# Kernel optimization log

Hardware: AMD Instinct MI355X
Metric: run time of the kernel (lower is better)

Reference implementation:

```python
import jax, jax.numpy as jnp
import numpy as np

N_NODES = 100000
N_EDGES = 1600000
IN_C, HID_C, OUT_C = 128, 128, 64


def setup_inputs() -> dict:
    key = jax.random.key(0)
    k1, k2, k3, k4 = jax.random.split(key, 4)
    x = jax.random.normal(k1, (N_NODES, IN_C), dtype=jnp.float32)
    edge_index = jax.random.randint(k2, (2, N_EDGES), 0, N_NODES, dtype=jnp.int32)
    # Glorot-ish init for linear weights, zero bias (PyG GCNConv default bias=0)
    W1 = jax.random.normal(k3, (IN_C, HID_C), dtype=jnp.float32) / np.sqrt(IN_C)
    b1 = jnp.zeros((HID_C,), dtype=jnp.float32)
    W2 = jax.random.normal(k4, (HID_C, OUT_C), dtype=jnp.float32) / np.sqrt(HID_C)
    b2 = jnp.zeros((OUT_C,), dtype=jnp.float32)
    return {"x": x, "edge_index": edge_index, "W1": W1, "b1": b1, "W2": W2, "b2": b2}


def gcn_conv(x, edge_index, W, b, n_nodes):
    """PyG GCNConv: out = D^{-1/2} (A + I) D^{-1/2} (x W) + b."""
    h = x @ W  # [N, C_out]
    loop = jnp.arange(n_nodes, dtype=edge_index.dtype)
    src = jnp.concatenate([edge_index[0], loop])  # messages flow src -> dst
    dst = jnp.concatenate([edge_index[1], loop])
    # degree at destination nodes (includes self-loops)
    deg = jax.ops.segment_sum(jnp.ones_like(src, dtype=h.dtype), dst,
                              num_segments=n_nodes)
    dis = jnp.where(deg > 0, jax.lax.rsqrt(jnp.maximum(deg, 1e-12)), 0.0)
    norm = dis[src] * dis[dst]  # [E+N]
    msg = h[src] * norm[:, None]  # gather + scale
    out = jax.ops.segment_sum(msg, dst, num_segments=n_nodes)  # scatter-add
    return out + b


def reference(x, edge_index, W1, b1, W2, b2):
    h = jax.nn.relu(gcn_conv(x, edge_index, W1, b1, N_NODES))
    return gcn_conv(h, edge_index, W2, b2, N_NODES)
```

## Files before the change

### kernel.cpp

```cpp
#include <hip/hip_runtime.h>

#define N_NODES 100000
#define N_EDGES 1600000
#define IN_C 128
#define HID_C 128
#define OUT_C 64

#define SH 8
#define NBKT 391
#define CAP 4608
#define EPB 4096
#define EPT 16

typedef __attribute__((ext_vector_type(8))) short bf16x8;
typedef __attribute__((ext_vector_type(4))) float f32x4;

static __device__ __forceinline__ unsigned f2bf(float f) {
  union { float f; unsigned u; } v; v.f = f;
  unsigned r = v.u + 0x7fffu + ((v.u >> 16) & 1u);
  return r >> 16;
}
static __device__ __forceinline__ float bf2f(unsigned hu) {
  union { unsigned u; float f; } v; v.u = hu << 16; return v.f;
}
static __device__ __forceinline__ float bflo(unsigned u) {
  union { unsigned u; float f; } v; v.u = u << 16; return v.f;
}
static __device__ __forceinline__ float bfhi(unsigned u) {
  union { unsigned u; float f; } v; v.u = u & 0xffff0000u; return v.f;
}


__global__ __launch_bounds__(256) void k_partA(const int* __restrict__ src,
                                               const int* __restrict__ dst,
                                               int* __restrict__ bcnt,
                                               unsigned* __restrict__ tmp, int e) {
  __shared__ unsigned stage[EPB];
  __shared__ unsigned short bid[EPB];
  __shared__ int hist[NBKT];
  __shared__ int lstart[NBKT];
  __shared__ int base[NBKT];
  __shared__ int ps[256];
  const int t = threadIdx.x;
  const int e0 = blockIdx.x * EPB;
  const int m = (e0 + EPB < e ? EPB : e - e0);

  for (int i = t; i < NBKT; i += 256) hist[i] = 0;
  __syncthreads();

  int rsrc[EPT], rdst[EPT];
#pragma unroll
  for (int i = 0; i < EPT; ++i) {
    int idx = e0 + i * 256 + t;
    if (idx < e) {
      rsrc[i] = src[idx];
      rdst[i] = dst[idx];
      atomicAdd(&hist[rdst[i] >> SH], 1);
    }
  }
  __syncthreads();

  int a0 = (2 * t < NBKT) ? hist[2 * t] : 0;
  int a1 = (2 * t + 1 < NBKT) ? hist[2 * t + 1] : 0;
  ps[t] = a0 + a1;
  __syncthreads();
  for (int off = 1; off < 256; off <<= 1) {
    int add = (t >= off) ? ps[t - off] : 0;
    __syncthreads();
    ps[t] += add;
    __syncthreads();
  }
  int ex = ps[t] - (a0 + a1);
  if (2 * t < NBKT) lstart[2 * t] = ex;
  if (2 * t + 1 < NBKT) lstart[2 * t + 1] = ex + a0;

  for (int i = t; i < NBKT; i += 256) {
    int h = hist[i];
    base[i] = h ? atomicAdd(&bcnt[i], h) : 0;
    hist[i] = 0;
  }
  __syncthreads();

#pragma unroll
  for (int i = 0; i < EPT; ++i) {
    int idx = e0 + i * 256 + t;
    if (idx < e) {
      int d = rdst[i];
      int b = d >> SH;
      int pos = lstart[b] + atomicAdd(&hist[b], 1);
      stage[pos] = (unsigned)rsrc[i] | ((unsigned)(d & 255) << 17);
      bid[pos] = (unsigned short)b;
    }
  }
  __syncthreads();

  for (int pos = t; pos < m; pos += 256) {
    int b = bid[pos];
    int slot = base[b] + (pos - lstart[b]);
    if (slot < CAP)
      tmp[(size_t)b * CAP + slot] = stage[pos];
  }
}

__global__ __launch_bounds__(256) void k_cntb(const unsigned* __restrict__ tmp,
                                              const int* __restrict__ bcnt,
                                              int* __restrict__ cnt, int n) {
  __shared__ int h[256];
  const int b = blockIdx.x, t = threadIdx.x;
  h[t] = 0;
  __syncthreads();
  int m = bcnt[b];
  if (m > CAP) m = CAP;
  for (int j = t; j < m; j += 256)
    atomicAdd(&h[tmp[(size_t)b * CAP + j] >> 17], 1);
  __syncthreads();
  int node = (b << SH) + t;
  if (node < n) cnt[node] = h[t];
}

__global__ void k_scan_block(const int* __restrict__ cnt, int* __restrict__ rowptr,
                             int* __restrict__ bsums, float* __restrict__ dis, int n) {
  __shared__ int s[256];
  int t = threadIdx.x;
  int i = blockIdx.x * 256 + t;
  int v = (i < n) ? cnt[i] : 0;
  if (i < n) dis[i] = rsqrtf((float)(v + 1));
  s[t] = v;
  __syncthreads();
  for (int off = 1; off < 256; off <<= 1) {
    int add = (t >= off) ? s[t - off] : 0;
    __syncthreads();
    s[t] += add;
    __syncthreads();
  }
  if (i < n) rowptr[i] = s[t] - v;
  if (t == 255) bsums[blockIdx.x] = s[255];
}

__global__ void k_scan_sums(int* __restrict__ bsums, int nb) {
  __shared__ int s[512];
  int t = threadIdx.x;
  int v = (t < nb) ? bsums[t] : 0;
  s[t] = v;
  __syncthreads();
  for (int off = 1; off < 512; off <<= 1) {
    int add = (t >= off) ? s[t - off] : 0;
    __syncthreads();
    s[t] += add;
    __syncthreads();
  }
  if (t < nb) bsums[t] = s[t] - v;
}

__global__ void k_add_off(int* __restrict__ rowptr, const int* __restrict__ bsums,
                          int n, int e) {
  int i = blockIdx.x * blockDim.x + threadIdx.x;
  if (i < n) rowptr[i] += bsums[i >> 8];
  else if (i == n) rowptr[n] = e;
}

__global__ __launch_bounds__(256) void k_partB(const unsigned* __restrict__ tmp,
                                               const int* __restrict__ bcnt,
                                               const int* __restrict__ rowptr,
                                               int* __restrict__ col, int n) {
  __shared__ int cur[256];
  const int b = blockIdx.x;
  const int t = threadIdx.x;
  const int node = (b << SH) + t;
  cur[t] = (node < n) ? rowptr[node] : 0;
  __syncthreads();
  int m = bcnt[b];
  if (m > CAP) m = CAP;
  for (int j = t; j < m; j += 256) {
    unsigned v = tmp[(size_t)b * CAP + j];
    int pos = atomicAdd(&cur[v >> 17], 1);
    col[pos] = (int)(v & 0x1FFFFu);
  }
}


__global__ void k_prepW(const float* __restrict__ W1, const float* __restrict__ W2,
                        unsigned short* __restrict__ W1h, unsigned short* __restrict__ W1l,
                        unsigned short* __restrict__ W2h, unsigned short* __restrict__ W2l) {
  int i = blockIdx.x * blockDim.x + threadIdx.x;
  if (i < IN_C * HID_C) {
    int k = i >> 7, c = i & 127;
    float w = W1[i];
    unsigned hi = f2bf(w);
    W1h[c * 128 + k] = (unsigned short)hi;
    W1l[c * 128 + k] = (unsigned short)f2bf(w - bf2f(hi));
  }
  int j = i - IN_C * HID_C;
  if (j >= 0 && j < HID_C * OUT_C) {
    int k = j >> 6, c = j & 63;
    float w = W2[j];
    unsigned hi = f2bf(w);
    W2h[c * 128 + k] = (unsigned short)hi;
    W2l[c * 128 + k] = (unsigned short)f2bf(w - bf2f(hi));
  }
}


__global__ __launch_bounds__(256) void k_mfma1(const float* __restrict__ X,
                                               const unsigned short* __restrict__ Wh,
                                               const unsigned short* __restrict__ Wl,
                                               const float* __restrict__ dis,
                                               unsigned short* __restrict__ Hs, int n) {
  __shared__ unsigned short xs[64 * 136];
  const int t = threadIdx.x;
  const int w = t >> 6, l = t & 63;
  const int lr = l & 15, lk = (l >> 4) * 8;
  const int row0 = blockIdx.x * 64;

  bf16x8 Bh[2][4], Bl[2][4];
#pragma unroll
  for (int c2 = 0; c2 < 2; ++c2)
#pragma unroll
    for (int kb = 0; kb < 4; ++kb) {
      int colw = w * 32 + c2 * 16 + lr;
      Bh[c2][kb] = *(const bf16x8*)&Wh[(size_t)colw * 128 + kb * 32 + lk];
      Bl[c2][kb] = *(const bf16x8*)&Wl[(size_t)colw * 128 + kb * 32 + lk];
    }

  for (int i = t; i < 64 * 32; i += 256) {
    int r = i >> 5, q = i & 31;
    float4 v = make_float4(0.f, 0.f, 0.f, 0.f);
    if (row0 + r < n) v = ((const float4*)(X + (size_t)(row0 + r) * IN_C))[q];
    unsigned p0 = f2bf(v.x) | (f2bf(v.y) << 16);
    unsigned p1 = f2bf(v.z) | (f2bf(v.w) << 16);
    *(uint2*)&xs[r * 136 + q * 4] = make_uint2(p0, p1);
  }
  __syncthreads();

#pragma unroll
  for (int rst = 0; rst < 4; ++rst) {
    bf16x8 a[4];
#pragma unroll
    for (int kb = 0; kb < 4; ++kb)
      a[kb] = *(const bf16x8*)&xs[(rst * 16 + lr) * 136 + kb * 32 + lk];
    f32x4 acc0 = (f32x4){0.f, 0.f, 0.f, 0.f};
    f32x4 acc1 = (f32x4){0.f, 0.f, 0.f, 0.f};
#pragma unroll
    for (int kb = 0; kb < 4; ++kb) {
      acc0 = __builtin_amdgcn_mfma_f32_16x16x32_bf16(a[kb], Bh[0][kb], acc0, 0, 0, 0);
      acc1 = __builtin_amdgcn_mfma_f32_16x16x32_bf16(a[kb], Bh[1][kb], acc1, 0, 0, 0);
      acc0 = __builtin_amdgcn_mfma_f32_16x16x32_bf16(a[kb], Bl[0][kb], acc0, 0, 0, 0);
      acc1 = __builtin_amdgcn_mfma_f32_16x16x32_bf16(a[kb], Bl[1][kb], acc1, 0, 0, 0);
    }
    const int rbase = row0 + rst * 16 + (l >> 4) * 4;
    float dv[4];
#pragma unroll
    for (int j = 0; j < 4; ++j) dv[j] = (rbase + j < n) ? dis[rbase + j] : 0.f;
#pragma unroll
    for (int c2 = 0; c2 < 2; ++c2) {
      int colw = w * 32 + c2 * 16 + lr;
      const f32x4& acc = c2 ? acc1 : acc0;
#pragma unroll
      for (int j = 0; j < 4; ++j) {
        int row = rbase + j;
        if (row < n) Hs[(size_t)row * HID_C + colw] = (unsigned short)f2bf(acc[j] * dv[j]);
      }
    }
  }
}


__global__ __launch_bounds__(256) void k_mfma2(const unsigned* __restrict__ G,
                                               const unsigned short* __restrict__ Wh,
                                               const unsigned short* __restrict__ Wl,
                                               const float* __restrict__ dis,
                                               unsigned short* __restrict__ Hs, int n) {
  __shared__ unsigned short xs[64 * 136];
  const int t = threadIdx.x;
  const int w = t >> 6, l = t & 63;
  const int lr = l & 15, lk = (l >> 4) * 8;
  const int row0 = blockIdx.x * 64;

  bf16x8 Bh[4], Bl[4];
#pragma unroll
  for (int kb = 0; kb < 4; ++kb) {
    int colw = w * 16 + lr;
    Bh[kb] = *(const bf16x8*)&Wh[(size_t)colw * 128 + kb * 32 + lk];
    Bl[kb] = *(const bf16x8*)&Wl[(size_t)colw * 128 + kb * 32 + lk];
  }

  for (int i = t; i < 64 * 32; i += 256) {
    int r = i >> 5, q = i & 31;
    uint2 v = make_uint2(0u, 0u);
    if (row0 + r < n) v = *(const uint2*)&G[(size_t)(row0 + r) * 64 + q * 2];
    *(uint2*)&xs[r * 136 + q * 4] = v;
  }
  __syncthreads();

#pragma unroll
  for (int rst = 0; rst < 4; ++rst) {
    bf16x8 a[4];
#pragma unroll
    for (int kb = 0; kb < 4; ++kb)
      a[kb] = *(const bf16x8*)&xs[(rst * 16 + lr) * 136 + kb * 32 + lk];
    f32x4 acc = (f32x4){0.f, 0.f, 0.f, 0.f};
#pragma unroll
    for (int kb = 0; kb < 4; ++kb) {
      acc = __builtin_amdgcn_mfma_f32_16x16x32_bf16(a[kb], Bh[kb], acc, 0, 0, 0);
      acc = __builtin_amdgcn_mfma_f32_16x16x32_bf16(a[kb], Bl[kb], acc, 0, 0, 0);
    }
    const int rbase = row0 + rst * 16 + (l >> 4) * 4;
    const int colw = w * 16 + lr;
#pragma unroll
    for (int j = 0; j < 4; ++j) {
      int row = rbase + j;
      if (row < n) Hs[(size_t)row * OUT_C + colw] =
          (unsigned short)f2bf(acc[j] * dis[row]);
    }
  }
}


__global__ __launch_bounds__(256) void k_agg128(const unsigned* __restrict__ Hs,
                                                const int* __restrict__ rowptr,
                                                const int* __restrict__ col,
                                                const float* __restrict__ dis,
                                                const float* __restrict__ bias,
                                                unsigned* __restrict__ G, int n) {
  const int node = (blockIdx.x * blockDim.x + threadIdx.x) >> 6;
  const int lane = threadIdx.x & 63;
  if (node >= n) return;
  unsigned u = Hs[(size_t)node * 64 + lane];
  float a0 = bflo(u), a1 = bfhi(u);
  int j = rowptr[node];
  const int end = rowptr[node + 1];
  for (; j + 8 <= end; j += 8) {
    int s0 = col[j], s1 = col[j + 1], s2 = col[j + 2], s3 = col[j + 3];
    int s4 = col[j + 4], s5 = col[j + 5], s6 = col[j + 6], s7 = col[j + 7];
    unsigned u0 = Hs[(size_t)s0 * 64 + lane];
    unsigned u1 = Hs[(size_t)s1 * 64 + lane];
    unsigned u2 = Hs[(size_t)s2 * 64 + lane];
    unsigned u3 = Hs[(size_t)s3 * 64 + lane];
    unsigned u4 = Hs[(size_t)s4 * 64 + lane];
    unsigned u5 = Hs[(size_t)s5 * 64 + lane];
    unsigned u6 = Hs[(size_t)s6 * 64 + lane];
    unsigned u7 = Hs[(size_t)s7 * 64 + lane];
    a0 += ((bflo(u0) + bflo(u1)) + (bflo(u2) + bflo(u3))) +
          ((bflo(u4) + bflo(u5)) + (bflo(u6) + bflo(u7)));
    a1 += ((bfhi(u0) + bfhi(u1)) + (bfhi(u2) + bfhi(u3))) +
          ((bfhi(u4) + bfhi(u5)) + (bfhi(u6) + bfhi(u7)));
  }
  for (; j + 4 <= end; j += 4) {
    int s0 = col[j], s1 = col[j + 1], s2 = col[j + 2], s3 = col[j + 3];
    unsigned u0 = Hs[(size_t)s0 * 64 + lane];
    unsigned u1 = Hs[(size_t)s1 * 64 + lane];
    unsigned u2 = Hs[(size_t)s2 * 64 + lane];
    unsigned u3 = Hs[(size_t)s3 * 64 + lane];
    a0 += (bflo(u0) + bflo(u1)) + (bflo(u2) + bflo(u3));
    a1 += (bfhi(u0) + bfhi(u1)) + (bfhi(u2) + bfhi(u3));
  }
  for (; j < end; ++j) {
    unsigned uu = Hs[(size_t)col[j] * 64 + lane];
    a0 += bflo(uu);
    a1 += bfhi(uu);
  }
  const float di = dis[node];
  const int c = lane * 2;
  float r0 = fmaxf(fmaf(a0, di, bias[c]), 0.f);
  float r1 = fmaxf(fmaf(a1, di, bias[c + 1]), 0.f);
  G[(size_t)node * 64 + lane] = f2bf(r0) | (f2bf(r1) << 16);
}

__global__ __launch_bounds__(256) void k_agg64(const unsigned* __restrict__ Hs,
                                               const int* __restrict__ rowptr,
                                               const int* __restrict__ col,
                                               const float* __restrict__ dis,
                                               const float* __restrict__ bias,
                                               float* __restrict__ out, int n) {
  const int node = (blockIdx.x * blockDim.x + threadIdx.x) >> 5;
  const int l = threadIdx.x & 31;
  if (node >= n) return;
  unsigned u = Hs[(size_t)node * 32 + l];
  float a0 = bflo(u), a1 = bfhi(u);
  int j = rowptr[node];
  const int end = rowptr[node + 1];
  for (; j + 8 <= end; j += 8) {
    int s0 = col[j], s1 = col[j + 1], s2 = col[j + 2], s3 = col[j + 3];
    int s4 = col[j + 4], s5 = col[j + 5], s6 = col[j + 6], s7 = col[j + 7];
    unsigned u0 = Hs[(size_t)s0 * 32 + l];
    unsigned u1 = Hs[(size_t)s1 * 32 + l];
    unsigned u2 = Hs[(size_t)s2 * 32 + l];
    unsigned u3 = Hs[(size_t)s3 * 32 + l];
    unsigned u4 = Hs[(size_t)s4 * 32 + l];
    unsigned u5 = Hs[(size_t)s5 * 32 + l];
    unsigned u6 = Hs[(size_t)s6 * 32 + l];
    unsigned u7 = Hs[(size_t)s7 * 32 + l];
    a0 += ((bflo(u0) + bflo(u1)) + (bflo(u2) + bflo(u3))) +
          ((bflo(u4) + bflo(u5)) + (bflo(u6) + bflo(u7)));
    a1 += ((bfhi(u0) + bfhi(u1)) + (bfhi(u2) + bfhi(u3))) +
          ((bfhi(u4) + bfhi(u5)) + (bfhi(u6) + bfhi(u7)));
  }
  for (; j + 4 <= end; j += 4) {
    int s0 = col[j], s1 = col[j + 1], s2 = col[j + 2], s3 = col[j + 3];
    unsigned u0 = Hs[(size_t)s0 * 32 + l];
    unsigned u1 = Hs[(size_t)s1 * 32 + l];
    unsigned u2 = Hs[(size_t)s2 * 32 + l];
    unsigned u3 = Hs[(size_t)s3 * 32 + l];
    a0 += (bflo(u0) + bflo(u1)) + (bflo(u2) + bflo(u3));
    a1 += (bfhi(u0) + bfhi(u1)) + (bfhi(u2) + bfhi(u3));
  }
  for (; j < end; ++j) {
    unsigned uu = Hs[(size_t)col[j] * 32 + l];
    a0 += bflo(uu);
    a1 += bfhi(uu);
  }
  const float di = dis[node];
  const int c = l * 2;
  float r0 = fmaf(a0, di, bias[c]);
  float r1 = fmaf(a1, di, bias[c + 1]);
  *(float2*)&out[(size_t)node * 64 + c] = make_float2(r0, r1);
}


extern "C" void kernel_launch(void* const* d_in, const int* in_sizes, int n_in,
                              void* d_out, int out_size, void* d_ws, size_t ws_size,
                              hipStream_t stream) {
  const float* x  = (const float*)d_in[0];
  const int*   ei = (const int*)d_in[1];
  const float* W1 = (const float*)d_in[2];
  const float* b1 = (const float*)d_in[3];
  const float* W2 = (const float*)d_in[4];
  const float* b2 = (const float*)d_in[5];
  float* out = (float*)d_out;

  const int N = N_NODES, E = N_EDGES;
  const int* esrc = ei;
  const int* edst = ei + E;

  char* w = (char*)d_ws;
  auto alloc = [&](size_t bytes) -> char* {
    char* p = w;
    w += (bytes + 255) & ~(size_t)255;
    return p;
  };
  float* dis          = (float*)alloc((size_t)N * 4);
  int* rowptr         = (int*)alloc((size_t)(N + 1) * 4);
  int* cnt            = (int*)alloc((size_t)N * 4);
  int* bcnt           = (int*)alloc((size_t)NBKT * 4);
  int* bsums          = (int*)alloc(512 * 4);
  int* col            = (int*)alloc((size_t)E * 4);
  unsigned* tmp       = (unsigned*)alloc((size_t)NBKT * CAP * 4);
  unsigned short* h1s = (unsigned short*)alloc((size_t)N * HID_C * 2);
  unsigned* g1        = (unsigned*)alloc((size_t)N * (HID_C / 2) * 4);
  unsigned short* h2s = (unsigned short*)alloc((size_t)N * OUT_C * 2);
  unsigned short* W1h = (unsigned short*)alloc((size_t)IN_C * HID_C * 2);
  unsigned short* W1l = (unsigned short*)alloc((size_t)IN_C * HID_C * 2);
  unsigned short* W2h = (unsigned short*)alloc((size_t)HID_C * OUT_C * 2);
  unsigned short* W2l = (unsigned short*)alloc((size_t)HID_C * OUT_C * 2);

  const int nb = (N + 255) / 256;

  hipMemsetAsync(bcnt, 0, (size_t)NBKT * 4, stream);
  k_partA<<<(E + EPB - 1) / EPB, 256, 0, stream>>>(esrc, edst, bcnt, tmp, E);
  k_cntb<<<NBKT, 256, 0, stream>>>(tmp, bcnt, cnt, N);
  k_scan_block<<<nb, 256, 0, stream>>>(cnt, rowptr, bsums, dis, N);
  k_scan_sums<<<1, 512, 0, stream>>>(bsums, nb);
  k_add_off<<<(N + 1 + 255) / 256, 256, 0, stream>>>(rowptr, bsums, N, E);
  k_partB<<<NBKT, 256, 0, stream>>>(tmp, bcnt, rowptr, col, N);
  k_prepW<<<(IN_C * HID_C + HID_C * OUT_C + 255) / 256, 256, 0, stream>>>(
      W1, W2, W1h, W1l, W2h, W2l);

  k_mfma1<<<(N + 63) / 64, 256, 0, stream>>>(x, W1h, W1l, dis, h1s, N);
  k_agg128<<<(N * 64 + 255) / 256, 256, 0, stream>>>((const unsigned*)h1s, rowptr, col,
                                                     dis, b1, g1, N);
  k_mfma2<<<(N + 63) / 64, 256, 0, stream>>>(g1, W2h, W2l, dis, h2s, N);
  k_agg64<<<(N * 32 + 255) / 256, 256, 0, stream>>>((const unsigned*)h2s, rowptr, col,
                                                    dis, b2, out, N);
}
```

Measured before the change: 208.3 us.

## Split edges across wavefront quarters with 16-byte gathers; fuse count and block scan

The aggregation kernels now split each node's edge list across four 16-lane groups. Each lane gathers a 16-byte (agg128) or 8-byte (agg64) slice of a neighbour row, and the partial sums are combined with cross-lane shuffles. agg64 also moves from 32 to 64 lanes per node. This aims to issue fewer, wider memory requests per neighbour row and give more gathers in flight per wavefront. Separately, the per-bucket degree count and the block-level prefix scan are merged into one kernel, since bucket size equals scan block size, which drops a launch and the cnt buffer. The cost is more registers for accumulators, a shuffle reduction, and idle lanes for low-degree nodes.

```diff
diff --git a/kernel.cpp b/kernel.cpp
--- a/kernel.cpp
+++ b/kernel.cpp
@@ -102,10 +102,13 @@
   }
 }
 
-__global__ __launch_bounds__(256) void k_cntb(const unsigned* __restrict__ tmp,
-                                              const int* __restrict__ bcnt,
-                                              int* __restrict__ cnt, int n) {
+__global__ __launch_bounds__(256) void k_cnt_scan(const unsigned* __restrict__ tmp,
+                                                  const int* __restrict__ bcnt,
+                                                  int* __restrict__ rowptr,
+                                                  int* __restrict__ bsums,
+                                                  float* __restrict__ dis, int n) {
   __shared__ int h[256];
+  __shared__ int s[256];
   const int b = blockIdx.x, t = threadIdx.x;
   h[t] = 0;
   __syncthreads();
@@ -114,17 +117,9 @@
   for (int j = t; j < m; j += 256)
     atomicAdd(&h[tmp[(size_t)b * CAP + j] >> 17], 1);
   __syncthreads();
-  int node = (b << SH) + t;
-  if (node < n) cnt[node] = h[t];
-}
-
-__global__ void k_scan_block(const int* __restrict__ cnt, int* __restrict__ rowptr,
-                             int* __restrict__ bsums, float* __restrict__ dis, int n) {
-  __shared__ int s[256];
-  int t = threadIdx.x;
-  int i = blockIdx.x * 256 + t;
-  int v = (i < n) ? cnt[i] : 0;
-  if (i < n) dis[i] = rsqrtf((float)(v + 1));
+  const int node = (b << SH) + t;
+  int v = (node < n) ? h[t] : 0;
+  if (node < n) dis[node] = rsqrtf((float)(v + 1));
   s[t] = v;
   __syncthreads();
   for (int off = 1; off < 256; off <<= 1) {
@@ -133,8 +128,8 @@
     s[t] += add;
     __syncthreads();
   }
-  if (i < n) rowptr[i] = s[t] - v;
-  if (t == 255) bsums[blockIdx.x] = s[255];
+  if (node < n) rowptr[node] = s[t] - v;
+  if (t == 255) bsums[b] = s[255];
 }
 
 __global__ void k_scan_sums(int* __restrict__ bsums, int nb) {
@@ -325,45 +320,58 @@
   const int node = (blockIdx.x * blockDim.x + threadIdx.x) >> 6;
   const int lane = threadIdx.x & 63;
   if (node >= n) return;
-  unsigned u = Hs[(size_t)node * 64 + lane];
-  float a0 = bflo(u), a1 = bfhi(u);
-  int j = rowptr[node];
-  const int end = rowptr[node + 1];
+  const int g = lane >> 4, q = lane & 15;
+  float a0 = 0.f, a1 = 0.f, a2 = 0.f, a3 = 0.f, a4 = 0.f, a5 = 0.f, a6 = 0.f, a7 = 0.f;
+  const int beg = rowptr[node], end = rowptr[node + 1];
+  int j = beg + g;
   for (; j + 8 <= end; j += 8) {
-    int s0 = col[j], s1 = col[j + 1], s2 = col[j + 2], s3 = col[j + 3];
-    int s4 = col[j + 4], s5 = col[j + 5], s6 = col[j + 6], s7 = col[j + 7];
-    unsigned u0 = Hs[(size_t)s0 * 64 + lane];
-    unsigned u1 = Hs[(size_t)s1 * 64 + lane];
-    unsigned u2 = Hs[(size_t)s2 * 64 + lane];
-    unsigned u3 = Hs[(size_t)s3 * 64 + lane];
-    unsigned u4 = Hs[(size_t)s4 * 64 + lane];
-    unsigned u5 = Hs[(size_t)s5 * 64 + lane];
-    unsigned u6 = Hs[(size_t)s6 * 64 + lane];
-    unsigned u7 = Hs[(size_t)s7 * 64 + lane];
-    a0 += ((bflo(u0) + bflo(u1)) + (bflo(u2) + bflo(u3))) +
-          ((bflo(u4) + bflo(u5)) + (bflo(u6) + bflo(u7)));
-    a1 += ((bfhi(u0) + bfhi(u1)) + (bfhi(u2) + bfhi(u3))) +
-          ((bfhi(u4) + bfhi(u5)) + (bfhi(u6) + bfhi(u7)));
-  }
-  for (; j + 4 <= end; j += 4) {
-    int s0 = col[j], s1 = col[j + 1], s2 = col[j + 2], s3 = col[j + 3];
-    unsigned u0 = Hs[(size_t)s0 * 64 + lane];
-    unsigned u1 = Hs[(size_t)s1 * 64 + lane];
-    unsigned u2 = Hs[(size_t)s2 * 64 + lane];
-    unsigned u3 = Hs[(size_t)s3 * 64 + lane];
-    a0 += (bflo(u0) + bflo(u1)) + (bflo(u2) + bflo(u3));
-    a1 += (bfhi(u0) + bfhi(u1)) + (bfhi(u2) + bfhi(u3));
-  }
-  for (; j < end; ++j) {
-    unsigned uu = Hs[(size_t)col[j] * 64 + lane];
-    a0 += bflo(uu);
-    a1 += bfhi(uu);
-  }
+    int s0 = col[j], s1 = col[j + 4];
+    uint4 v0 = *(const uint4*)&Hs[(size_t)s0 * 64 + q * 4];
+    uint4 v1 = *(const uint4*)&Hs[(size_t)s1 * 64 + q * 4];
+    a0 += bflo(v0.x) + bflo(v1.x); a1 += bfhi(v0.x) + bfhi(v1.x);
+    a2 += bflo(v0.y) + bflo(v1.y); a3 += bfhi(v0.y) + bfhi(v1.y);
+    a4 += bflo(v0.z) + bflo(v1.z); a5 += bfhi(v0.z) + bfhi(v1.z);
+    a6 += bflo(v0.w) + bflo(v1.w); a7 += bfhi(v0.w) + bfhi(v1.w);
+  }
+  for (; j < end; j += 4) {
+    int s = col[j];
+    uint4 v = *(const uint4*)&Hs[(size_t)s * 64 + q * 4];
+    a0 += bflo(v.x); a1 += bfhi(v.x);
+    a2 += bflo(v.y); a3 += bfhi(v.y);
+    a4 += bflo(v.z); a5 += bfhi(v.z);
+    a6 += bflo(v.w); a7 += bfhi(v.w);
+  }
+  a0 += __shfl_xor(a0, 16, 64); a0 += __shfl_xor(a0, 32, 64);
+  a1 += __shfl_xor(a1, 16, 64); a1 += __shfl_xor(a1, 32, 64);
+  a2 += __shfl_xor(a2, 16, 64); a2 += __shfl_xor(a2, 32, 64);
+  a3 += __shfl_xor(a3, 16, 64); a3 += __shfl_xor(a3, 32, 64);
+  a4 += __shfl_xor(a4, 16, 64); a4 += __shfl_xor(a4, 32, 64);
+  a5 += __shfl_xor(a5, 16, 64); a5 += __shfl_xor(a5, 32, 64);
+  a6 += __shfl_xor(a6, 16, 64); a6 += __shfl_xor(a6, 32, 64);
+  a7 += __shfl_xor(a7, 16, 64); a7 += __shfl_xor(a7, 32, 64);
+  uint4 sv = *(const uint4*)&Hs[(size_t)node * 64 + q * 4];
   const float di = dis[node];
-  const int c = lane * 2;
-  float r0 = fmaxf(fmaf(a0, di, bias[c]), 0.f);
-  float r1 = fmaxf(fmaf(a1, di, bias[c + 1]), 0.f);
-  G[(size_t)node * 64 + lane] = f2bf(r0) | (f2bf(r1) << 16);
+  const int c0 = q * 8;
+  float2 b0 = *(const float2*)&bias[c0];
+  float2 b1 = *(const float2*)&bias[c0 + 2];
+  float2 b2 = *(const float2*)&bias[c0 + 4];
+  float2 b3 = *(const float2*)&bias[c0 + 6];
+  float r0 = fmaxf(fmaf(a0 + bflo(sv.x), di, b0.x), 0.f);
+  float r1 = fmaxf(fmaf(a1 + bfhi(sv.x), di, b0.y), 0.f);
+  float r2 = fmaxf(fmaf(a2 + bflo(sv.y), di, b1.x), 0.f);
+  float r3 = fmaxf(fmaf(a3 + bfhi(sv.y), di, b1.y), 0.f);
+  float r4 = fmaxf(fmaf(a4 + bflo(sv.z), di, b2.x), 0.f);
+  float r5 = fmaxf(fmaf(a5 + bfhi(sv.z), di, b2.y), 0.f);
+  float r6 = fmaxf(fmaf(a6 + bflo(sv.w), di, b3.x), 0.f);
+  float r7 = fmaxf(fmaf(a7 + bfhi(sv.w), di, b3.y), 0.f);
+  if (g == 0) {
+    uint4 pk;
+    pk.x = f2bf(r0) | (f2bf(r1) << 16);
+    pk.y = f2bf(r2) | (f2bf(r3) << 16);
+    pk.z = f2bf(r4) | (f2bf(r5) << 16);
+    pk.w = f2bf(r6) | (f2bf(r7) << 16);
+    *(uint4*)&G[(size_t)node * 64 + q * 4] = pk;
+  }
 }
 
 __global__ __launch_bounds__(256) void k_agg64(const unsigned* __restrict__ Hs,
@@ -372,48 +380,43 @@
                                                const float* __restrict__ dis,
                                                const float* __restrict__ bias,
                                                float* __restrict__ out, int n) {
-  const int node = (blockIdx.x * blockDim.x + threadIdx.x) >> 5;
-  const int l = threadIdx.x & 31;
+  const int node = (blockIdx.x * blockDim.x + threadIdx.x) >> 6;
+  const int lane = threadIdx.x & 63;
   if (node >= n) return;
-  unsigned u = Hs[(size_t)node * 32 + l];
-  float a0 = bflo(u), a1 = bfhi(u);
-  int j = rowptr[node];
-  const int end = rowptr[node + 1];
+  const int g = lane >> 4, q = lane & 15;
+  float a0 = 0.f, a1 = 0.f, a2 = 0.f, a3 = 0.f;
+  const int beg = rowptr[node], end = rowptr[node + 1];
+  int j = beg + g;
   for (; j + 8 <= end; j += 8) {
-    int s0 = col[j], s1 = col[j + 1], s2 = col[j + 2], s3 = col[j + 3];
-    int s4 = col[j + 4], s5 = col[j + 5], s6 = col[j + 6], s7 = col[j + 7];
-    unsigned u0 = Hs[(size_t)s0 * 32 + l];
-    unsigned u1 = Hs[(size_t)s1 * 32 + l];
-    unsigned u2 = Hs[(size_t)s2 * 32 + l];
-    unsigned u3 = Hs[(size_t)s3 * 32 + l];
-    unsigned u4 = Hs[(size_t)s4 * 32 + l];
-    unsigned u5 = Hs[(size_t)s5 * 32 + l];
-    unsigned u6 = Hs[(size_t)s6 * 32 + l];
-    unsigned u7 = Hs[(size_t)s7 * 32 + l];
-    a0 += ((bflo(u0) + bflo(u1)) + (bflo(u2) + bflo(u3))) +
-          ((bflo(u4) + bflo(u5)) + (bflo(u6) + bflo(u7)));
-    a1 += ((bfhi(u0) + bfhi(u1)) + (bfhi(u2) + bfhi(u3))) +
-          ((bfhi(u4) + bfhi(u5)) + (bfhi(u6) + bfhi(u7)));
-  }
-  for (; j + 4 <= end; j += 4) {
-    int s0 = col[j], s1 = col[j + 1], s2 = col[j + 2], s3 = col[j + 3];
-    unsigned u0 = Hs[(size_t)s0 * 32 + l];
-    unsigned u1 = Hs[(size_t)s1 * 32 + l];
-    unsigned u2 = Hs[(size_t)s2 * 32 + l];
-    unsigned u3 = Hs[(size_t)s3 * 32 + l];
-    a0 += (bflo(u0) + bflo(u1)) + (bflo(u2) + bflo(u3));
-    a1 += (bfhi(u0) + bfhi(u1)) + (bfhi(u2) + bfhi(u3));
-  }
-  for (; j < end; ++j) {
-    unsigned uu = Hs[(size_t)col[j] * 32 + l];
-    a0 += bflo(uu);
-    a1 += bfhi(uu);
-  }
+    int s0 = col[j], s1 = col[j + 4];
+    uint2 v0 = *(const uint2*)&Hs[(size_t)s0 * 32 + q * 2];
+    uint2 v1 = *(const uint2*)&Hs[(size_t)s1 * 32 + q * 2];
+    a0 += bflo(v0.x) + bflo(v1.x); a1 += bfhi(v0.x) + bfhi(v1.x);
+    a2 += bflo(v0.y) + bflo(v1.y); a3 += bfhi(v0.y) + bfhi(v1.y);
+  }
+  for (; j < end; j += 4) {
+    int s = col[j];
+    uint2 v = *(const uint2*)&Hs[(size_t)s * 32 + q * 2];
+    a0 += bflo(v.x); a1 += bfhi(v.x);
+    a2 += bflo(v.y); a3 += bfhi(v.y);
+  }
+  a0 += __shfl_xor(a0, 16, 64); a0 += __shfl_xor(a0, 32, 64);
+  a1 += __shfl_xor(a1, 16, 64); a1 += __shfl_xor(a1, 32, 64);
+  a2 += __shfl_xor(a2, 16, 64); a2 += __shfl_xor(a2, 32, 64);
+  a3 += __shfl_xor(a3, 16, 64); a3 += __shfl_xor(a3, 32, 64);
+  uint2 sv = *(const uint2*)&Hs[(size_t)node * 32 + q * 2];
   const float di = dis[node];
-  const int c = l * 2;
-  float r0 = fmaf(a0, di, bias[c]);
-  float r1 = fmaf(a1, di, bias[c + 1]);
-  *(float2*)&out[(size_t)node * 64 + c] = make_float2(r0, r1);
+  const int c0 = q * 4;
+  float2 b0 = *(const float2*)&bias[c0];
+  float2 b1 = *(const float2*)&bias[c0 + 2];
+  if (g == 0) {
+    float4 r;
+    r.x = fmaf(a0 + bflo(sv.x), di, b0.x);
+    r.y = fmaf(a1 + bfhi(sv.x), di, b0.y);
+    r.z = fmaf(a2 + bflo(sv.y), di, b1.x);
+    r.w = fmaf(a3 + bfhi(sv.y), di, b1.y);
+    *(float4*)&out[(size_t)node * 64 + c0] = r;
+  }
 }
 
 
@@ -440,7 +443,6 @@
   };
   float* dis          = (float*)alloc((size_t)N * 4);
   int* rowptr         = (int*)alloc((size_t)(N + 1) * 4);
-  int* cnt            = (int*)alloc((size_t)N * 4);
   int* bcnt           = (int*)alloc((size_t)NBKT * 4);
   int* bsums          = (int*)alloc(512 * 4);
   int* col            = (int*)alloc((size_t)E * 4);
@@ -453,13 +455,10 @@
   unsigned short* W2h = (unsigned short*)alloc((size_t)HID_C * OUT_C * 2);
   unsigned short* W2l = (unsigned short*)alloc((size_t)HID_C * OUT_C * 2);
 
-  const int nb = (N + 255) / 256;
-
   hipMemsetAsync(bcnt, 0, (size_t)NBKT * 4, stream);
   k_partA<<<(E + EPB - 1) / EPB, 256, 0, stream>>>(esrc, edst, bcnt, tmp, E);
-  k_cntb<<<NBKT, 256, 0, stream>>>(tmp, bcnt, cnt, N);
-  k_scan_block<<<nb, 256, 0, stream>>>(cnt, rowptr, bsums, dis, N);
-  k_scan_sums<<<1, 512, 0, stream>>>(bsums, nb);
+  k_cnt_scan<<<NBKT, 256, 0, stream>>>(tmp, bcnt, rowptr, bsums, dis, N);
+  k_scan_sums<<<1, 512, 0, stream>>>(bsums, NBKT);
   k_add_off<<<(N + 1 + 255) / 256, 256, 0, stream>>>(rowptr, bsums, N, E);
   k_partB<<<NBKT, 256, 0, stream>>>(tmp, bcnt, rowptr, col, N);
   k_prepW<<<(IN_C * HID_C + HID_C * OUT_C + 255) / 256, 256, 0, stream>>>(
@@ -469,6 +468,6 @@
   k_agg128<<<(N * 64 + 255) / 256, 256, 0, stream>>>((const unsigned*)h1s, rowptr, col,
                                                      dis, b1, g1, N);
   k_mfma2<<<(N + 63) / 64, 256, 0, stream>>>(g1, W2h, W2l, dis, h2s, N);
-  k_agg64<<<(N * 32 + 255) / 256, 256, 0, stream>>>((const unsigned*)h2s, rowptr, col,
+  k_agg64<<<(N * 64 + 255) / 256, 256, 0, stream>>>((const unsigned*)h2s, rowptr, col,
                                                     dis, b2, out, N);
 }
```

Result: slower. 220.5 us (+5.9%).

## Fuse CSR build into bucket-scan plus single per-bucket count/scan/scatter kernel

Applied to the files above, without the earlier changes.

Replaces five CSR-construction kernels (per-bucket count, block scan, sums scan, offset add, scatter) with a small bucket-level exclusive scan and one per-bucket kernel. That kernel histograms the bucket's nodes, computes degree normalization and rowptr, and scatters column indices in place. This cuts kernel launches and a global round trip of counts and rowptr. Edges per block in the partition kernel are also halved to spread the work over more blocks. One risk: rowptr[n] now uses the clamped bucket totals rather than E.

```diff
diff --git a/kernel.cpp b/kernel.cpp
--- a/kernel.cpp
+++ b/kernel.cpp
@@ -9,8 +9,8 @@
 #define SH 8
 #define NBKT 391
 #define CAP 4608
-#define EPB 4096
-#define EPT 16
+#define EPB 2048
+#define EPT 8
 
 typedef __attribute__((ext_vector_type(8))) short bf16x8;
 typedef __attribute__((ext_vector_type(4))) float f32x4;
@@ -102,29 +102,46 @@
   }
 }
 
-__global__ __launch_bounds__(256) void k_cntb(const unsigned* __restrict__ tmp,
-                                              const int* __restrict__ bcnt,
-                                              int* __restrict__ cnt, int n) {
+__global__ __launch_bounds__(512) void k_bscan(const int* __restrict__ bcnt,
+                                               int* __restrict__ bstart) {
+  __shared__ int s[512];
+  const int t = threadIdx.x;
+  int v = 0;
+  if (t < NBKT) {
+    v = bcnt[t];
+    if (v > CAP) v = CAP;
+  }
+  s[t] = v;
+  __syncthreads();
+  for (int off = 1; off < 512; off <<= 1) {
+    int add = (t >= off) ? s[t - off] : 0;
+    __syncthreads();
+    s[t] += add;
+    __syncthreads();
+  }
+  if (t <= NBKT) bstart[t] = s[t] - v;
+}
+
+__global__ __launch_bounds__(256) void k_bucket(const unsigned* __restrict__ tmp,
+                                                const int* __restrict__ bcnt,
+                                                const int* __restrict__ bstart,
+                                                int* __restrict__ rowptr,
+                                                int* __restrict__ col,
+                                                float* __restrict__ dis, int n) {
   __shared__ int h[256];
+  __shared__ int s[256];
   const int b = blockIdx.x, t = threadIdx.x;
   h[t] = 0;
   __syncthreads();
   int m = bcnt[b];
   if (m > CAP) m = CAP;
+  const unsigned* tb = tmp + (size_t)b * CAP;
   for (int j = t; j < m; j += 256)
-    atomicAdd(&h[tmp[(size_t)b * CAP + j] >> 17], 1);
-  __syncthreads();
-  int node = (b << SH) + t;
-  if (node < n) cnt[node] = h[t];
-}
-
-__global__ void k_scan_block(const int* __restrict__ cnt, int* __restrict__ rowptr,
-                             int* __restrict__ bsums, float* __restrict__ dis, int n) {
-  __shared__ int s[256];
-  int t = threadIdx.x;
-  int i = blockIdx.x * 256 + t;
-  int v = (i < n) ? cnt[i] : 0;
-  if (i < n) dis[i] = rsqrtf((float)(v + 1));
+    atomicAdd(&h[tb[j] >> 17], 1);
+  __syncthreads();
+  const int node = (b << SH) + t;
+  const int v = h[t];
+  if (node < n) dis[node] = rsqrtf((float)(v + 1));
   s[t] = v;
   __syncthreads();
   for (int off = 1; off < 256; off <<= 1) {
@@ -133,48 +150,17 @@
     s[t] += add;
     __syncthreads();
   }
-  if (i < n) rowptr[i] = s[t] - v;
-  if (t == 255) bsums[blockIdx.x] = s[255];
-}
-
-__global__ void k_scan_sums(int* __restrict__ bsums, int nb) {
-  __shared__ int s[512];
-  int t = threadIdx.x;
-  int v = (t < nb) ? bsums[t] : 0;
-  s[t] = v;
-  __syncthreads();
-  for (int off = 1; off < 512; off <<= 1) {
-    int add = (t >= off) ? s[t - off] : 0;
-    __syncthreads();
-    s[t] += add;
-    __syncthreads();
-  }
-  if (t < nb) bsums[t] = s[t] - v;
-}
-
-__global__ void k_add_off(int* __restrict__ rowptr, const int* __restrict__ bsums,
-                          int n, int e) {
-  int i = blockIdx.x * blockDim.x + threadIdx.x;
-  if (i < n) rowptr[i] += bsums[i >> 8];
-  else if (i == n) rowptr[n] = e;
-}
-
-__global__ __launch_bounds__(256) void k_partB(const unsigned* __restrict__ tmp,
-                                               const int* __restrict__ bcnt,
-                                               const int* __restrict__ rowptr,
-                                               int* __restrict__ col, int n) {
-  __shared__ int cur[256];
-  const int b = blockIdx.x;
-  const int t = threadIdx.x;
-  const int node = (b << SH) + t;
-  cur[t] = (node < n) ? rowptr[node] : 0;
-  __syncthreads();
-  int m = bcnt[b];
-  if (m > CAP) m = CAP;
+  const int base = bstart[b];
+  const int ex = s[t] - v;
+  if (node < n) rowptr[node] = base + ex;
+  if (b == 0 && t == 0) rowptr[n] = bstart[NBKT];
+  __syncthreads();
+  h[t] = base + ex;
+  __syncthreads();
   for (int j = t; j < m; j += 256) {
-    unsigned v = tmp[(size_t)b * CAP + j];
-    int pos = atomicAdd(&cur[v >> 17], 1);
-    col[pos] = (int)(v & 0x1FFFFu);
+    unsigned u = tb[j];
+    int pos = atomicAdd(&h[u >> 17], 1);
+    col[pos] = (int)(u & 0x1FFFFu);
   }
 }
 
@@ -440,9 +426,8 @@
   };
   float* dis          = (float*)alloc((size_t)N * 4);
   int* rowptr         = (int*)alloc((size_t)(N + 1) * 4);
-  int* cnt            = (int*)alloc((size_t)N * 4);
   int* bcnt           = (int*)alloc((size_t)NBKT * 4);
-  int* bsums          = (int*)alloc(512 * 4);
+  int* bstart         = (int*)alloc((size_t)(NBKT + 1) * 4);
   int* col            = (int*)alloc((size_t)E * 4);
   unsigned* tmp       = (unsigned*)alloc((size_t)NBKT * CAP * 4);
   unsigned short* h1s = (unsigned short*)alloc((size_t)N * HID_C * 2);
@@ -453,15 +438,10 @@
   unsigned short* W2h = (unsigned short*)alloc((size_t)HID_C * OUT_C * 2);
   unsigned short* W2l = (unsigned short*)alloc((size_t)HID_C * OUT_C * 2);
 
-  const int nb = (N + 255) / 256;
-
   hipMemsetAsync(bcnt, 0, (size_t)NBKT * 4, stream);
   k_partA<<<(E + EPB - 1) / EPB, 256, 0, stream>>>(esrc, edst, bcnt, tmp, E);
-  k_cntb<<<NBKT, 256, 0, stream>>>(tmp, bcnt, cnt, N);
-  k_scan_block<<<nb, 256, 0, stream>>>(cnt, rowptr, bsums, dis, N);
-  k_scan_sums<<<1, 512, 0, stream>>>(bsums, nb);
-  k_add_off<<<(N + 1 + 255) / 256, 256, 0, stream>>>(rowptr, bsums, N, E);
-  k_partB<<<NBKT, 256, 0, stream>>>(tmp, bcnt, rowptr, col, N);
+  k_bscan<<<1, 512, 0, stream>>>(bcnt, bstart);
+  k_bucket<<<NBKT, 256, 0, stream>>>(tmp, bcnt, bstart, rowptr, col, dis, N);
   k_prepW<<<(IN_C * HID_C + HID_C * OUT_C + 255) / 256, 256, 0, stream>>>(
       W1, W2, W1h, W1l, W2h, W2l);
 
```

Result: no change. 209.9 us, median of 2 (+0.8%).
